# Optimization experiments

Hardware: AMD Instinct MI355X
Metric: run time of the kernel (lower is better)

The kernel has to match this reference:

```python
import jax, jax.numpy as jnp
import numpy as np

SEQ_LEN, BATCH, INPUT_SIZE, HIDDEN = 512, 64, 256, 1024


def setup_inputs() -> dict:
    key = jax.random.key(0)
    ks = jax.random.split(key, 17)
    inp = {"x": jax.random.normal(ks[0], (SEQ_LEN, BATCH, INPUT_SIZE), dtype=jnp.float32)}
    # 8 Linear layers: odd-numbered take x (in=INPUT_SIZE), even-numbered take h (in=HIDDEN).
    sx = 1.0 / np.sqrt(INPUT_SIZE)
    sh = 1.0 / np.sqrt(HIDDEN)
    for i in range(1, 9):
        fan_in, scale = (INPUT_SIZE, sx) if i % 2 == 1 else (HIDDEN, sh)
        inp[f"W{i}"] = jax.random.uniform(ks[2 * i - 1], (fan_in, HIDDEN), jnp.float32, -scale, scale)
        inp[f"b{i}"] = jax.random.uniform(ks[2 * i], (HIDDEN,), jnp.float32, -scale, scale)
    return inp


def reference(x, W1, b1, W2, b2, W3, b3, W4, b4, W5, b5, W6, b6, W7, b7, W8, b8):
    # Gate order matching the torch module: out1(f-like)=lin1/lin2, out2(i)=lin3/lin4,
    # out3(o)=lin5/lin6, cand=lin7/lin8.  Fuse the 4 input-side GEMMs into one big GEMM
    # over all timesteps, and the 4 hidden-side GEMMs into one per-step GEMM.
    Wx = jnp.concatenate([W1, W3, W5, W7], axis=1)            # (I, 4H)
    bx = jnp.concatenate([b1, b3, b5, b7], axis=0)            # (4H,)
    Wh = jnp.concatenate([W2, W4, W6, W8], axis=1)            # (H, 4H)
    bh = jnp.concatenate([b2, b4, b6, b8], axis=0)            # (4H,)

    H = W2.shape[0]
    xg = jnp.einsum('sbi,ig->sbg', x, Wx) + bx + bh           # (S, B, 4H)

    def step(carry, xg_t):
        h, c = carry                                          # (B, H) each
        g = xg_t + h @ Wh                                     # (B, 4H)
        f = jax.nn.sigmoid(g[:, 0 * H:1 * H])
        i = jax.nn.sigmoid(g[:, 1 * H:2 * H])
        o = jax.nn.sigmoid(g[:, 2 * H:3 * H])
        cand = jnp.tanh(g[:, 3 * H:4 * H])
        c = f * c + i * cand
        h = o * jnp.tanh(c)
        return (h, c), h

    B = x.shape[1]
    h0 = jnp.zeros((B, H), dtype=x.dtype)
    c0 = jnp.zeros((B, H), dtype=x.dtype)
    (h, c), h_seq = jax.lax.scan(step, (h0, c0), xg)
    # Torch module returns (h_seq, (h, c)) with h,c leading dim 1.
    return h_seq, (h[None], c[None])
```

## Files before the change

### kernel.cpp

```cpp
#include <hip/hip_runtime.h>


#define OFF_XB    0ul
#define OFF_WXP   16777216ul
#define OFF_WHP   18874368ul
#define OFF_BIAS  27262976ul
#define OFF_HBUF  27279360ul
#define OFF_FLG   27541504ul

typedef __attribute__((ext_vector_type(8))) __bf16 bf16x8;
typedef __attribute__((ext_vector_type(4))) float  floatx4;

struct KPtrs { const float* p[17]; };

__device__ __forceinline__ unsigned short f2bf(float f) {
  unsigned int u = __float_as_uint(f);
  u += 0x7fffu + ((u >> 16) & 1u);
  return (unsigned short)(u >> 16);
}

__device__ __forceinline__ bf16x8 ld16(const unsigned short* p) {
  return *(const bf16x8*)p;
}

__device__ __forceinline__ bf16x8 ldsys16(const unsigned short* p) {
  unsigned long long a =
      __hip_atomic_load((const unsigned long long*)p,       __ATOMIC_RELAXED, __HIP_MEMORY_SCOPE_AGENT);
  unsigned long long b =
      __hip_atomic_load((const unsigned long long*)(p + 4), __ATOMIC_RELAXED, __HIP_MEMORY_SCOPE_AGENT);
  unsigned long long arr[2] = {a, b};
  bf16x8 r;
  __builtin_memcpy(&r, arr, 16);
  return r;
}

__device__ __forceinline__ float fsig(float x) {
  return __builtin_amdgcn_rcpf(1.f + __expf(-x));
}
__device__ __forceinline__ float ftanh(float x) {
  return 1.f - 2.f * __builtin_amdgcn_rcpf(1.f + __expf(2.f * x));
}

__global__ void pack_kernel(KPtrs P, unsigned char* ws) {
  unsigned short* xb   = (unsigned short*)(ws + OFF_XB);
  unsigned short* wxp  = (unsigned short*)(ws + OFF_WXP);
  unsigned short* whp  = (unsigned short*)(ws + OFF_WHP);
  float*          bias = (float*)(ws + OFF_BIAS);
  unsigned int*   hb32 = (unsigned int*)(ws + OFF_HBUF);
  int*            flg  = (int*)(ws + OFF_FLG);
  const float* x = P.p[0];

  const long tid = (long)blockIdx.x * blockDim.x + threadIdx.x;
  const long nth = (long)gridDim.x * blockDim.x;

  for (long e = tid; e < 8388608l; e += nth)
    xb[e] = f2bf(x[e]);
  for (long e = tid; e < 1048576l; e += nth) {
    int c = (int)(e >> 8), i = (int)(e & 255);
    int gg = c >> 10, j = c & 1023;
    wxp[e] = f2bf(P.p[1 + 4 * gg][i * 1024 + j]);
  }
  for (long e = tid; e < 4194304l; e += nth) {
    int c = (int)(e >> 10), k = (int)(e & 1023);
    int gg = c >> 10, j = c & 1023;
    long dst = ((long)c << 10) | (long)(k ^ ((c & 7) << 3));
    whp[dst] = f2bf(P.p[3 + 4 * gg][k * 1024 + j]);
  }
  for (long e = tid; e < 4096l; e += nth) {
    int gg = (int)(e >> 10), j = (int)(e & 1023);
    bias[e] = P.p[2 + 4 * gg][j] + P.p[4 + 4 * gg][j];
  }
  for (long e = tid; e < 65536l; e += nth)
    __hip_atomic_store(&hb32[e], 0u, __ATOMIC_RELAXED, __HIP_MEMORY_SCOPE_AGENT);
  for (long e = tid; e < 128l; e += nth)
    __hip_atomic_store(&flg[e], -1, __ATOMIC_RELAXED, __HIP_MEMORY_SCOPE_AGENT);
}

__global__ void __launch_bounds__(256, 1)
lstm_kernel(const unsigned char* __restrict__ ws, float* __restrict__ out) {
  const unsigned short* xb   = (const unsigned short*)(ws + OFF_XB);
  const unsigned short* wxp  = (const unsigned short*)(ws + OFF_WXP);
  const unsigned short* whp  = (const unsigned short*)(ws + OFF_WHP);
  const float*          bias = (const float*)(ws + OFF_BIAS);
  unsigned short*       hbuf = (unsigned short*)(ws + OFF_HBUF);
  int*                  flg  = (int*)(ws + OFF_FLG);

  const int tid = threadIdx.x;
  const int wv = tid >> 6, lane = tid & 63;
  const int r = lane & 15, q = lane >> 4;
  const int s = blockIdx.x & 63, g = blockIdx.x >> 6;

  __shared__ unsigned short whl[65536];
  __shared__ float pc[4][4][64][4];

  for (int ch = tid; ch < 8192; ch += 256) {
    const int le = ch * 8;
    const int rl = le >> 10, k8 = le & 1023;
    const int cg = (rl >> 4) * 1024 + s * 16 + (rl & 15);
    *(bf16x8*)&whl[le] = ld16(whp + (long)cg * 1024 + k8);
  }

  bf16x8 wxf[4][2];
#pragma unroll
  for (int nt = 0; nt < 4; ++nt) {
    const int c = nt * 1024 + s * 16 + r;
#pragma unroll
    for (int kk = 0; kk < 2; ++kk)
      wxf[nt][kk] = ld16(wxp + (long)c * 256 + wv * 64 + kk * 32 + q * 8);
  }

  const int ej = tid & 15, eb = tid >> 4;
  const int lidx = ej | ((eb >> 2) << 4), rg = eb & 3;
  float bs[4];
#pragma unroll
  for (int gt = 0; gt < 4; ++gt) bs[gt] = bias[gt * 1024 + s * 16 + ej];

  const unsigned short* xa0 = xb + (long)(g * 32 + r) * 256 + q * 8;
  const int rs = (r & 7) << 3;
  const unsigned long long* fl64 = (const unsigned long long*)flg;
  const int fidx = g * 32 + (lane & 31);

  float cst[2] = {0.f, 0.f};
  __syncthreads();

  for (int t = 0; t < 512; ++t) {
    unsigned long long fv =
        __hip_atomic_load(&fl64[fidx], __ATOMIC_RELAXED, __HIP_MEMORY_SCOPE_AGENT);

    const unsigned short* xaT = xa0 + (long)t * 16384;
    bf16x8 xv[2][2];
#pragma unroll
    for (int kk = 0; kk < 2; ++kk) {
      xv[0][kk] = ld16(xaT + wv * 64 + kk * 32);
      xv[1][kk] = ld16(xaT + 16 * 256 + wv * 64 + kk * 32);
    }

    floatx4 acc[2][4];
#pragma unroll
    for (int mt = 0; mt < 2; ++mt)
#pragma unroll
      for (int nt = 0; nt < 4; ++nt) acc[mt][nt] = (floatx4){0.f, 0.f, 0.f, 0.f};

#pragma unroll
    for (int kk = 0; kk < 2; ++kk)
#pragma unroll
      for (int nt = 0; nt < 4; ++nt) {
        acc[0][nt] = __builtin_amdgcn_mfma_f32_16x16x32_bf16(xv[0][kk], wxf[nt][kk], acc[0][nt], 0, 0, 0);
        acc[1][nt] = __builtin_amdgcn_mfma_f32_16x16x32_bf16(xv[1][kk], wxf[nt][kk], acc[1][nt], 0, 0, 0);
      }

    {
      const int need = t - 1;
      while (!(((int)(unsigned int)fv >= need) && ((int)(unsigned int)(fv >> 32) >= need) ?
               __all(1) : __all(0))) {
        __builtin_amdgcn_s_sleep(1);
        fv = __hip_atomic_load(&fl64[fidx], __ATOMIC_RELAXED, __HIP_MEMORY_SCOPE_AGENT);
      }
    }
    asm volatile("" ::: "memory");

    const unsigned short* ha =
        hbuf + (long)((t - 1) & 1) * 65536 + ((long)g * 32 + r) * 1024 + q * 8;
    bf16x8 hv0[8], hv1[8];
#pragma unroll
    for (int kk = 0; kk < 8; ++kk) {
      const int k0 = wv * 256 + kk * 32;
      hv0[kk] = ldsys16(ha + k0);
      hv1[kk] = ldsys16(ha + 16 * 1024 + k0);
    }

#pragma unroll
    for (int kk = 0; kk < 8; ++kk) {
      bf16x8 wb[4];
      const int el = wv * 256 + ((kk * 32 + q * 8) ^ rs);
#pragma unroll
      for (int nt = 0; nt < 4; ++nt)
        wb[nt] = *(const bf16x8*)&whl[(nt * 16 + r) * 1024 + el];
#pragma unroll
      for (int nt = 0; nt < 4; ++nt) {
        acc[0][nt] = __builtin_amdgcn_mfma_f32_16x16x32_bf16(hv0[kk], wb[nt], acc[0][nt], 0, 0, 0);
        acc[1][nt] = __builtin_amdgcn_mfma_f32_16x16x32_bf16(hv1[kk], wb[nt], acc[1][nt], 0, 0, 0);
      }
    }

    float hvv[2];
#pragma unroll
    for (int e = 0; e < 2; ++e) {
      __syncthreads();
#pragma unroll
      for (int nt = 0; nt < 4; ++nt)
        *(floatx4*)(&pc[wv][nt][lane][0]) = acc[e][nt];
      __syncthreads();

      float gs[4];
#pragma unroll
      for (int gt = 0; gt < 4; ++gt)
        gs[gt] = bs[gt] + pc[0][gt][lidx][rg] + pc[1][gt][lidx][rg] +
                 pc[2][gt][lidx][rg] + pc[3][gt][lidx][rg];
      const float f = fsig(gs[0]), ii = fsig(gs[1]), o = fsig(gs[2]);
      const float cd = ftanh(gs[3]);
      cst[e] = f * cst[e] + ii * cd;
      hvv[e] = o * ftanh(cst[e]);

      unsigned short hb16 = f2bf(hvv[e]);
      unsigned short nbv = (unsigned short)__shfl_xor((int)hb16, 1, 64);
      if ((ej & 1) == 0) {
        unsigned int pv = (unsigned int)hb16 | ((unsigned int)nbv << 16);
        unsigned int* hp = (unsigned int*)(hbuf + (long)(t & 1) * 65536 +
            (long)(g * 32 + e * 16 + eb) * 1024 + s * 16 + ej);
        __hip_atomic_store(hp, pv, __ATOMIC_RELAXED, __HIP_MEMORY_SCOPE_AGENT);
      }

      const long ob = (long)(g * 32 + e * 16 + eb) * 1024 + s * 16 + ej;
      out[(long)t * 65536 + ob] = hvv[e];
      if (t == 511) {
        out[33554432l + ob] = hvv[e];
        out[33619968l + ob] = cst[e];
      }
    }

    __syncthreads();
    if (tid == 0)
      __hip_atomic_store(&flg[blockIdx.x], t, __ATOMIC_RELAXED, __HIP_MEMORY_SCOPE_AGENT);
  }
}

extern "C" void kernel_launch(void* const* d_in, const int* in_sizes, int n_in,
                              void* d_out, int out_size, void* d_ws, size_t ws_size,
                              hipStream_t stream) {
  (void)in_sizes; (void)n_in; (void)out_size; (void)ws_size;
  KPtrs P;
  for (int i = 0; i < 17; ++i) P.p[i] = (const float*)d_in[i];
  pack_kernel<<<dim3(2048), dim3(256), 0, stream>>>(P, (unsigned char*)d_ws);
  lstm_kernel<<<dim3(128), dim3(256), 0, stream>>>((const unsigned char*)d_ws, (float*)d_out);
}
```

Baseline: 3.702 ms.

## Use per-wave step flags and publish h before output stores

Replaces the per-block step flag with per-wave flags: each wave signals completion itself after draining its h stores with a waitcnt, rather than waiting on a block barrier and one thread. The accumulator spill to shared memory for both row tiles now happens in one pass, so the per-step barriers drop from five to two, and the shared buffer doubles in size. The big output stores move after the flag publish so consumers are not held up by them. Spinning now polls without sleep and reads one flag per lane, which risks more memory traffic from polling.

```diff
diff --git a/kernel.cpp b/kernel.cpp
--- a/kernel.cpp
+++ b/kernel.cpp
@@ -6,7 +6,7 @@
 #define OFF_WHP   18874368ul
 #define OFF_BIAS  27262976ul
 #define OFF_HBUF  27279360ul
-#define OFF_FLG   27541504ul
+#define OFF_CNR   27541504ul
 
 typedef __attribute__((ext_vector_type(8))) __bf16 bf16x8;
 typedef __attribute__((ext_vector_type(4))) float  floatx4;
@@ -34,6 +34,10 @@
   return r;
 }
 
+__device__ __forceinline__ int lduc32(const int* p) {
+  return __hip_atomic_load(p, __ATOMIC_RELAXED, __HIP_MEMORY_SCOPE_AGENT);
+}
+
 __device__ __forceinline__ float fsig(float x) {
   return __builtin_amdgcn_rcpf(1.f + __expf(-x));
 }
@@ -47,7 +51,7 @@
   unsigned short* whp  = (unsigned short*)(ws + OFF_WHP);
   float*          bias = (float*)(ws + OFF_BIAS);
   unsigned int*   hb32 = (unsigned int*)(ws + OFF_HBUF);
-  int*            flg  = (int*)(ws + OFF_FLG);
+  int*            cnr  = (int*)(ws + OFF_CNR);
   const float* x = P.p[0];
 
   const long tid = (long)blockIdx.x * blockDim.x + threadIdx.x;
@@ -72,8 +76,8 @@
   }
   for (long e = tid; e < 65536l; e += nth)
     __hip_atomic_store(&hb32[e], 0u, __ATOMIC_RELAXED, __HIP_MEMORY_SCOPE_AGENT);
-  for (long e = tid; e < 128l; e += nth)
-    __hip_atomic_store(&flg[e], -1, __ATOMIC_RELAXED, __HIP_MEMORY_SCOPE_AGENT);
+  for (long e = tid; e < 512l; e += nth)
+    __hip_atomic_store(&cnr[e], -1, __ATOMIC_RELAXED, __HIP_MEMORY_SCOPE_AGENT);
 }
 
 __global__ void __launch_bounds__(256, 1)
@@ -83,7 +87,7 @@
   const unsigned short* whp  = (const unsigned short*)(ws + OFF_WHP);
   const float*          bias = (const float*)(ws + OFF_BIAS);
   unsigned short*       hbuf = (unsigned short*)(ws + OFF_HBUF);
-  int*                  flg  = (int*)(ws + OFF_FLG);
+  int*                  cnr  = (int*)(ws + OFF_CNR);
 
   const int tid = threadIdx.x;
   const int wv = tid >> 6, lane = tid & 63;
@@ -91,7 +95,7 @@
   const int s = blockIdx.x & 63, g = blockIdx.x >> 6;
 
   __shared__ unsigned short whl[65536];
-  __shared__ float pc[4][4][64][4];
+  __shared__ float pc[4][8][64][4];
 
   for (int ch = tid; ch < 8192; ch += 256) {
     const int le = ch * 8;
@@ -117,15 +121,14 @@
 
   const unsigned short* xa0 = xb + (long)(g * 32 + r) * 256 + q * 8;
   const int rs = (r & 7) << 3;
-  const unsigned long long* fl64 = (const unsigned long long*)flg;
-  const int fidx = g * 32 + (lane & 31);
+  const int cidx = g * 256 + (wv * 16 + (lane >> 2)) * 4 + (lane & 3);
+  const int pidx = g * 256 + s * 4 + wv;
 
   float cst[2] = {0.f, 0.f};
   __syncthreads();
 
   for (int t = 0; t < 512; ++t) {
-    unsigned long long fv =
-        __hip_atomic_load(&fl64[fidx], __ATOMIC_RELAXED, __HIP_MEMORY_SCOPE_AGENT);
+    int cv = lduc32(&cnr[cidx]);
 
     const unsigned short* xaT = xa0 + (long)t * 16384;
     bf16x8 xv[2][2];
@@ -149,14 +152,9 @@
         acc[1][nt] = __builtin_amdgcn_mfma_f32_16x16x32_bf16(xv[1][kk], wxf[nt][kk], acc[1][nt], 0, 0, 0);
       }
 
-    {
-      const int need = t - 1;
-      while (!(((int)(unsigned int)fv >= need) && ((int)(unsigned int)(fv >> 32) >= need) ?
-               __all(1) : __all(0))) {
-        __builtin_amdgcn_s_sleep(1);
-        fv = __hip_atomic_load(&fl64[fidx], __ATOMIC_RELAXED, __HIP_MEMORY_SCOPE_AGENT);
-      }
-    }
+    const int need = t - 1;
+    while (!__all(cv >= need))
+      cv = lduc32(&cnr[cidx]);
     asm volatile("" ::: "memory");
 
     const unsigned short* ha =
@@ -168,6 +166,7 @@
       hv0[kk] = ldsys16(ha + k0);
       hv1[kk] = ldsys16(ha + 16 * 1024 + k0);
     }
+    __builtin_amdgcn_sched_barrier(0);
 
 #pragma unroll
     for (int kk = 0; kk < 8; ++kk) {
@@ -183,25 +182,31 @@
       }
     }
 
+#pragma unroll
+    for (int mt = 0; mt < 2; ++mt)
+#pragma unroll
+      for (int nt = 0; nt < 4; ++nt)
+        *(floatx4*)(&pc[wv][mt * 4 + nt][lane][0]) = acc[mt][nt];
+    __syncthreads();
+
     float hvv[2];
 #pragma unroll
     for (int e = 0; e < 2; ++e) {
-      __syncthreads();
-#pragma unroll
-      for (int nt = 0; nt < 4; ++nt)
-        *(floatx4*)(&pc[wv][nt][lane][0]) = acc[e][nt];
-      __syncthreads();
-
       float gs[4];
 #pragma unroll
       for (int gt = 0; gt < 4; ++gt)
-        gs[gt] = bs[gt] + pc[0][gt][lidx][rg] + pc[1][gt][lidx][rg] +
-                 pc[2][gt][lidx][rg] + pc[3][gt][lidx][rg];
+        gs[gt] = bs[gt] + pc[0][e * 4 + gt][lidx][rg] + pc[1][e * 4 + gt][lidx][rg] +
+                 pc[2][e * 4 + gt][lidx][rg] + pc[3][e * 4 + gt][lidx][rg];
       const float f = fsig(gs[0]), ii = fsig(gs[1]), o = fsig(gs[2]);
       const float cd = ftanh(gs[3]);
       cst[e] = f * cst[e] + ii * cd;
       hvv[e] = o * ftanh(cst[e]);
-
+    }
+
+    __syncthreads();
+
+#pragma unroll
+    for (int e = 0; e < 2; ++e) {
       unsigned short hb16 = f2bf(hvv[e]);
       unsigned short nbv = (unsigned short)__shfl_xor((int)hb16, 1, 64);
       if ((ej & 1) == 0) {
@@ -210,7 +215,13 @@
             (long)(g * 32 + e * 16 + eb) * 1024 + s * 16 + ej);
         __hip_atomic_store(hp, pv, __ATOMIC_RELAXED, __HIP_MEMORY_SCOPE_AGENT);
       }
-
+    }
+    asm volatile("s_waitcnt vmcnt(0)" ::: "memory");
+    if (lane == 0)
+      __hip_atomic_store(&cnr[pidx], t, __ATOMIC_RELAXED, __HIP_MEMORY_SCOPE_AGENT);
+
+#pragma unroll
+    for (int e = 0; e < 2; ++e) {
       const long ob = (long)(g * 32 + e * 16 + eb) * 1024 + s * 16 + ej;
       out[(long)t * 65536 + ob] = hvv[e];
       if (t == 511) {
@@ -218,10 +229,6 @@
         out[33619968l + ob] = cst[e];
       }
     }
-
-    __syncthreads();
-    if (tid == 0)
-      __hip_atomic_store(&flg[blockIdx.x], t, __ATOMIC_RELAXED, __HIP_MEMORY_SCOPE_AGENT);
   }
 }
 
```

Result: slower. 3.956 ms (+6.8%).
